# Kernel tuning notes

Measured on AMD Instinct MI355X. Metric: run time of the kernel, lower is better.

The kernel has to match this reference:

```python
import jax, jax.numpy as jnp
import numpy as np

L, D, DH, NH, P = 12, 768, 64, 12, 16
B, H_IMG, W_IMG = 16, 384, 384
MAX_GRID = 64


def setup_inputs() -> dict:
    key = jax.random.key(0)
    ks = jax.random.split(key, 10)
    r = lambda k, shp: (0.02 * jax.random.normal(k, shp, dtype=jnp.float32))
    return {
        "x": jax.random.normal(ks[0], (B, 3, H_IMG, W_IMG), dtype=jnp.float32),
        "conv_w": r(ks[1], (D, 3, P, P)),
        "conv_b": jnp.zeros((D,), jnp.float32),
        "ln_w": jnp.ones((D,), jnp.float32),
        "ln_b": jnp.zeros((D,), jnp.float32),
        "pos_y_emb": r(ks[2], (MAX_GRID, D)),
        "pos_x_emb": r(ks[3], (MAX_GRID, D)),
        "mha_ln_w": jnp.ones((L, D), jnp.float32),
        "mha_ln_b": jnp.zeros((L, D), jnp.float32),
        "qw": r(ks[4], (L, D, D)),
        "kw": r(ks[5], (L, D, D)),
        "vw": r(ks[6], (L, D, D)),
        "ffn_ln_w": jnp.ones((L, D), jnp.float32),
        "ffn_ln_b": jnp.zeros((L, D), jnp.float32),
        "w1": r(ks[7], (L, D, 4 * D)),
        "b1": jnp.zeros((L, 4 * D), jnp.float32),
        "w2": r(ks[8], (L, 4 * D, D)),
        "b2": jnp.zeros((L, D), jnp.float32),
        "x_shift": 0,
        "y_shift": 0,
    }


def _ln(x, w, b):
    m = jnp.mean(x, axis=-1, keepdims=True)
    v = jnp.var(x, axis=-1, keepdims=True)
    return (x - m) * jax.lax.rsqrt(v + 1e-5) * w + b


def reference(x, conv_w, conv_b, ln_w, ln_b, pos_y_emb, pos_x_emb,
              mha_ln_w, mha_ln_b, qw, kw, vw,
              ffn_ln_w, ffn_ln_b, w1, b1, w2, b2, x_shift, y_shift):
    # patch embed: conv + relu, to NHWC, layernorm
    h = jax.lax.conv_general_dilated(x, conv_w, (P, P), 'VALID',
                                     dimension_numbers=('NCHW', 'OIHW', 'NCHW'))
    h = jax.nn.relu(h + conv_b[None, :, None, None])
    h = jnp.transpose(h, (0, 2, 3, 1))  # [B, GH, GW, D]
    h = _ln(h, ln_w, ln_b)
    b, gh, gw, d = h.shape
    n = gh * gw
    # 2D factorized positional embedding, shared layernorm
    pos = (pos_y_emb[jnp.arange(gh) + y_shift][:, None, :]
           + pos_x_emb[jnp.arange(gw) + x_shift][None, :, :])  # [GH, GW, D]
    pos = _ln(pos, ln_w, ln_b).reshape(1, n, d)
    pos_emb = jnp.broadcast_to(pos, (b, n, d))
    t = h.reshape(b, n, d) + pos_emb
    scale = 1.0 / jnp.sqrt(jnp.float32(DH))
    for i in range(L):
        # pre-LN MHA (no output projection, mask=None / pretrain=False)
        tl = _ln(t, mha_ln_w[i], mha_ln_b[i])
        q = (tl @ qw[i]).reshape(b, n, NH, DH).transpose(0, 2, 1, 3)
        k = (tl @ kw[i]).reshape(b, n, NH, DH).transpose(0, 2, 1, 3)
        v = (tl @ vw[i]).reshape(b, n, NH, DH).transpose(0, 2, 1, 3)
        attn = jax.nn.softmax(jnp.einsum('bhqd,bhkd->bhqk', q, k) * scale, axis=-1)
        o = jnp.einsum('bhqk,bhkd->bhqd', attn, v).transpose(0, 2, 1, 3).reshape(b, n, d)
        t = t + o
        fl = _ln(t, ffn_ln_w[i], ffn_ln_b[i])
        t = t + (jax.nn.relu(fl @ w1[i] + b1[i]) @ w2[i] + b2[i])
    return t, pos_emb
```

## Files before the change

kernel.cpp:

```cpp
#include <hip/hip_runtime.h>

typedef unsigned short u16;
typedef __attribute__((ext_vector_type(4))) float f32x4;
typedef __attribute__((ext_vector_type(8))) short s16x8;

__device__ __forceinline__ u16 f2bf(float f) {
    union { float f; unsigned u; } v; v.f = f;
    unsigned r = v.u + 0x7FFFu + ((v.u >> 16) & 1u);
    return (u16)(r >> 16);
}

__device__ __forceinline__ void gload_lds16(const u16* g, u16* l) {
    __builtin_amdgcn_global_load_lds(
        (const __attribute__((address_space(1))) unsigned int*)(g),
        (__attribute__((address_space(3))) unsigned int*)(l),
        16, 0, 0);
}

#define NTOK 9216
#define SEQ  576
#define DMODEL 768
#define DFF  3072
#define NHEAD 12
#define HDIM 64

__global__ __launch_bounds__(256) void convert_bf16_kernel(const float* __restrict__ in,
                                                           u16* __restrict__ out, int n) {
    for (int i = blockIdx.x * 256 + threadIdx.x; i < n; i += gridDim.x * 256)
        out[i] = f2bf(in[i]);
}

__global__ __launch_bounds__(256) void copy_f32_kernel(const float* __restrict__ in,
                                                       float* __restrict__ out, int n4) {
    const float4* a = (const float4*)in;
    float4* o = (float4*)out;
    for (int i = blockIdx.x * 256 + threadIdx.x; i < n4; i += gridDim.x * 256)
        o[i] = a[i];
}

__global__ __launch_bounds__(256) void im2col_kernel(const float* __restrict__ x,
                                                     u16* __restrict__ out) {
    int tok = blockIdx.x;
    int b = tok / SEQ, n = tok % SEQ;
    int gy = n / 24, gx = n % 24;
    int tid = threadIdx.x;
#pragma unroll
    for (int j = 0; j < 3; ++j) {
        int col = tid + j * 256;
        int c = col >> 8, py = (col >> 4) & 15, px = col & 15;
        float v = x[(size_t)((b * 3 + c) * 384 + gy * 16 + py) * 384 + gx * 16 + px];
        out[(size_t)tok * DMODEL + col] = f2bf(v);
    }
}

__global__ __launch_bounds__(256) void transpose_layer_kernel(
        const float* __restrict__ qw, const float* __restrict__ kw, const float* __restrict__ vw,
        const float* __restrict__ w1, const float* __restrict__ w2,
        u16* __restrict__ wTq, u16* __restrict__ wTk, u16* __restrict__ wTv,
        u16* __restrict__ w1T, u16* __restrict__ w2T) {
    int bid = blockIdx.x;
    const float* src; u16* dst; int Kd, Nd, tile;
    if (bid < 1728)      { int m = bid / 576; src = m == 0 ? qw : (m == 1 ? kw : vw);
                           dst = m == 0 ? wTq : (m == 1 ? wTk : wTv); Kd = 768; Nd = 768; tile = bid % 576; }
    else if (bid < 4032) { src = w1; dst = w1T; Kd = 768; Nd = 3072; tile = bid - 1728; }
    else                 { src = w2; dst = w2T; Kd = 3072; Nd = 768; tile = bid - 4032; }
    int ntx = Nd / 32;
    int tk = (tile / ntx) * 32, tn = (tile % ntx) * 32;
    __shared__ float ts[32][33];
    int tx = threadIdx.x & 31, ty = threadIdx.x >> 5;
#pragma unroll
    for (int j = 0; j < 32; j += 8)
        ts[ty + j][tx] = src[(size_t)(tk + ty + j) * Nd + tn + tx];
    __syncthreads();
#pragma unroll
    for (int j = 0; j < 32; j += 8)
        dst[(size_t)(tn + ty + j) * Kd + tk + tx] = f2bf(ts[tx][ty + j]);
}

__global__ __launch_bounds__(256) void ln_bf16_kernel(const float* __restrict__ X,
                                                      const float* __restrict__ w,
                                                      const float* __restrict__ b,
                                                      u16* __restrict__ Y) {
    int row = blockIdx.x, tid = threadIdx.x;
    const float* x = X + (size_t)row * DMODEL;
    float v0 = x[tid], v1 = x[tid + 256], v2 = x[tid + 512];
    float s = v0 + v1 + v2, sq = v0 * v0 + v1 * v1 + v2 * v2;
#pragma unroll
    for (int off = 32; off >= 1; off >>= 1) { s += __shfl_down(s, off); sq += __shfl_down(sq, off); }
    __shared__ float red[8];
    if ((tid & 63) == 0) { red[tid >> 6] = s; red[4 + (tid >> 6)] = sq; }
    __syncthreads();
    float S = red[0] + red[1] + red[2] + red[3];
    float Q = red[4] + red[5] + red[6] + red[7];
    float mean = S * (1.f / DMODEL);
    float var = Q * (1.f / DMODEL) - mean * mean;
    float inv = rsqrtf(var + 1e-5f);
    u16* y = Y + (size_t)row * DMODEL;
    y[tid]       = f2bf((v0 - mean) * inv * w[tid]       + b[tid]);
    y[tid + 256] = f2bf((v1 - mean) * inv * w[tid + 256] + b[tid + 256]);
    y[tid + 512] = f2bf((v2 - mean) * inv * w[tid + 512] + b[tid + 512]);
}

__global__ __launch_bounds__(256) void ln_add_pos_kernel(float* __restrict__ T,
                                                         const float* __restrict__ w,
                                                         const float* __restrict__ b,
                                                         const float* __restrict__ posln) {
    int row = blockIdx.x, tid = threadIdx.x;
    float* x = T + (size_t)row * DMODEL;
    const float* p = posln + (size_t)(row % SEQ) * DMODEL;
    float v0 = x[tid], v1 = x[tid + 256], v2 = x[tid + 512];
    float s = v0 + v1 + v2, sq = v0 * v0 + v1 * v1 + v2 * v2;
#pragma unroll
    for (int off = 32; off >= 1; off >>= 1) { s += __shfl_down(s, off); sq += __shfl_down(sq, off); }
    __shared__ float red[8];
    if ((tid & 63) == 0) { red[tid >> 6] = s; red[4 + (tid >> 6)] = sq; }
    __syncthreads();
    float S = red[0] + red[1] + red[2] + red[3];
    float Q = red[4] + red[5] + red[6] + red[7];
    float mean = S * (1.f / DMODEL);
    float var = Q * (1.f / DMODEL) - mean * mean;
    float inv = rsqrtf(var + 1e-5f);
    x[tid]       = (v0 - mean) * inv * w[tid]       + b[tid]       + p[tid];
    x[tid + 256] = (v1 - mean) * inv * w[tid + 256] + b[tid + 256] + p[tid + 256];
    x[tid + 512] = (v2 - mean) * inv * w[tid + 512] + b[tid + 512] + p[tid + 512];
}

__global__ __launch_bounds__(256) void pos_ln_kernel(const float* __restrict__ py,
                                                     const float* __restrict__ px,
                                                     const float* __restrict__ w,
                                                     const float* __restrict__ b,
                                                     const int* __restrict__ xs_p,
                                                     const int* __restrict__ ys_p,
                                                     float* __restrict__ posln,
                                                     float* __restrict__ out2) {
    int row = blockIdx.x;
    int gy = row / 24, gx = row % 24;
    int ys = ys_p[0], xs = xs_p[0];
    int tid = threadIdx.x;
    float v[3]; float s = 0.f, sq = 0.f;
#pragma unroll
    for (int j = 0; j < 3; ++j) {
        int c = tid + j * 256;
        v[j] = py[(size_t)(gy + ys) * DMODEL + c] + px[(size_t)(gx + xs) * DMODEL + c];
        s += v[j]; sq += v[j] * v[j];
    }
#pragma unroll
    for (int off = 32; off >= 1; off >>= 1) { s += __shfl_down(s, off); sq += __shfl_down(sq, off); }
    __shared__ float red[8];
    if ((tid & 63) == 0) { red[tid >> 6] = s; red[4 + (tid >> 6)] = sq; }
    __syncthreads();
    float S = red[0] + red[1] + red[2] + red[3];
    float Q = red[4] + red[5] + red[6] + red[7];
    float mean = S * (1.f / DMODEL);
    float var = Q * (1.f / DMODEL) - mean * mean;
    float inv = rsqrtf(var + 1e-5f);
#pragma unroll
    for (int j = 0; j < 3; ++j) {
        int c = tid + j * 256;
        float y = (v[j] - mean) * inv * w[c] + b[c];
        posln[(size_t)row * DMODEL + c] = y;
        for (int bb = 0; bb < 16; ++bb)
            out2[((size_t)bb * SEQ + row) * DMODEL + c] = y;
    }
}

#define EPI_CONV 0
#define EPI_QKV  1
#define EPI_FFN1 3
#define EPI_FFN2 4

template <int EPI>
__global__ __launch_bounds__(512, 4) void gemm3b(const u16* __restrict__ A,
                                                 const u16* __restrict__ Bt,
                                                 float* __restrict__ outF,
                                                 u16* __restrict__ outB,
                                                 u16* __restrict__ outB2,
                                                 u16* __restrict__ outB3,
                                                 const float* __restrict__ bias,
                                                 int lda, int N, int K) {
    __shared__ __align__(16) u16 lds[3 * 12288];
    const int tid = threadIdx.x;
    const int wave = tid >> 6, lane = tid & 63;
    const int c_lo = lane & 15, c_hi = lane >> 4;
    const int wm = wave >> 2, wn = wave & 3;
    const int m0 = blockIdx.x * 128, n0 = blockIdx.y * 256;
    const int NT = K >> 5;

    const int srow = tid >> 2;
    const int koff = ((tid & 3) * 8) ^ (((srow >> 1) & 3) << 3);
    const u16* pA = A  + (size_t)(m0 + srow) * lda + koff;
    const u16* pB = Bt + (size_t)(n0 + srow) * lda + koff;
    const size_t rstepB = (size_t)128 * lda;
    f32x4 acc[4][4] = {};

    auto stage = [&](int t) {
        u16* buf = lds + (t % 3) * 12288;
        int k0 = t << 5;
        gload_lds16(pA + k0, buf + tid * 8);
        gload_lds16(pB + k0, buf + 4096 + tid * 8);
        gload_lds16(pB + rstepB + k0, buf + 8192 + tid * 8);
    };

    stage(0); stage(1);
    asm volatile("s_waitcnt vmcnt(3)" ::: "memory");
    __builtin_amdgcn_s_barrier();
    __builtin_amdgcn_sched_barrier(0);

    const int sw = ((c_lo >> 1) & 3) << 3;
    const int colA = (c_hi * 8) ^ sw;

    for (int t = 0; t < NT; ++t) {
        if (t + 2 < NT) stage(t + 2);
        const u16* buf = lds + (t % 3) * 12288;
        s16x8 af[4], bf[4];
#pragma unroll
        for (int m = 0; m < 4; ++m)
            af[m] = *(const s16x8*)(buf + (wm * 64 + m * 16 + c_lo) * 32 + colA);
#pragma unroll
        for (int n = 0; n < 4; ++n)
            bf[n] = *(const s16x8*)(buf + 4096 + (wn * 64 + n * 16 + c_lo) * 32 + colA);
        asm volatile("s_waitcnt lgkmcnt(0)" ::: "memory");
        __builtin_amdgcn_sched_barrier(0);
        __builtin_amdgcn_s_setprio(1);
#pragma unroll
        for (int m = 0; m < 4; ++m)
#pragma unroll
            for (int n = 0; n < 4; ++n)
                acc[m][n] = __builtin_amdgcn_mfma_f32_16x16x32_bf16(af[m], bf[n], acc[m][n], 0, 0, 0);
        __builtin_amdgcn_s_setprio(0);
        if (t + 2 < NT)      { asm volatile("s_waitcnt vmcnt(3)" ::: "memory"); }
        else if (t + 1 < NT) { asm volatile("s_waitcnt vmcnt(0)" ::: "memory"); }
        __builtin_amdgcn_s_barrier();
        __builtin_amdgcn_sched_barrier(0);
    }

#pragma unroll
    for (int mf = 0; mf < 4; ++mf)
#pragma unroll
        for (int nf = 0; nf < 4; ++nf)
#pragma unroll
            for (int rr = 0; rr < 4; ++rr) {
                int grow = m0 + wm * 64 + mf * 16 + c_hi * 4 + rr;
                int gcol = n0 + wn * 64 + nf * 16 + c_lo;
                float v = acc[mf][nf][rr];
                if (EPI == EPI_CONV) {
                    v += bias[gcol]; v = fmaxf(v, 0.f);
                    outF[(size_t)grow * 768 + gcol] = v;
                } else if (EPI == EPI_QKV) {
                    int sel = n0 / 768;
                    int lcol = gcol - sel * 768;
                    if (sel == 0)      outB [(size_t)grow * 768 + lcol] = f2bf(v);
                    else if (sel == 1) outB2[(size_t)grow * 768 + lcol] = f2bf(v);
                    else {
                        int b = grow / SEQ, nt = grow % SEQ;
                        int h = lcol >> 6, dh = lcol & 63;
                        outB3[(size_t)(((b * NHEAD + h) << 6) + dh) * SEQ + nt] = f2bf(v);
                    }
                } else if (EPI == EPI_FFN1) {
                    v += bias[gcol]; v = fmaxf(v, 0.f);
                    outB[(size_t)grow * N + gcol] = f2bf(v);
                } else if (EPI == EPI_FFN2) {
                    outF[(size_t)grow * 768 + gcol] += v + bias[gcol];
                }
            }
}

__global__ __launch_bounds__(256) void attn_kernel(const u16* __restrict__ Qb,
                                                   const u16* __restrict__ Kb,
                                                   const u16* __restrict__ Vt,
                                                   float* __restrict__ T) {
    int bid = blockIdx.x;
    int qt = bid / 192, bh = bid % 192;
    int b = bh / NHEAD, h = bh % NHEAD;
    int q0 = qt * 64;
    const int tid = threadIdx.x, wave = tid >> 6, lane = tid & 63;
    const int c_lo = lane & 15, c_hi = lane >> 4;
    __shared__ __align__(16) u16 Qs[64][72];
    __shared__ __align__(16) u16 Ks[64][72];
    __shared__ __align__(16) u16 Vs[64][72];
    __shared__ __align__(16) u16 Ps[4][16][72];
#pragma unroll
    for (int i = 0; i < 2; ++i) {
        int c = i * 256 + tid, row = c >> 3, slot = (c & 7) * 8;
        *(s16x8*)&Qs[row][slot] =
            *(const s16x8*)(Qb + ((size_t)(b * SEQ + q0 + row) * DMODEL + h * HDIM + slot));
    }
    s16x8 kreg[2], vreg[2];
    {
#pragma unroll
        for (int i = 0; i < 2; ++i) {
            int c = i * 256 + tid, row = c >> 3, slot = (c & 7) * 8;
            kreg[i] = *(const s16x8*)(Kb + ((size_t)(b * SEQ + row) * DMODEL + h * HDIM + slot));
            vreg[i] = *(const s16x8*)(Vt + ((size_t)((b * NHEAD + h) * HDIM + row) * SEQ + slot));
        }
    }
    f32x4 o[4] = {};
    float mrun[4], lrun[4];
#pragma unroll
    for (int r = 0; r < 4; ++r) { mrun[r] = -1e30f; lrun[r] = 0.f; }
    for (int t2 = 0; t2 < 9; ++t2) {
        __builtin_amdgcn_s_barrier();
#pragma unroll
        for (int i = 0; i < 2; ++i) {
            int c = i * 256 + tid, row = c >> 3, slot = (c & 7) * 8;
            *(s16x8*)&Ks[row][slot] = kreg[i];
            *(s16x8*)&Vs[row][slot] = vreg[i];
        }
        asm volatile("s_waitcnt lgkmcnt(0)" ::: "memory");
        __builtin_amdgcn_s_barrier();
        __builtin_amdgcn_sched_barrier(0);
        if (t2 < 8) {
            int kv0 = (t2 + 1) * 64;
#pragma unroll
            for (int i = 0; i < 2; ++i) {
                int c = i * 256 + tid, row = c >> 3, slot = (c & 7) * 8;
                kreg[i] = *(const s16x8*)(Kb + ((size_t)(b * SEQ + kv0 + row) * DMODEL + h * HDIM + slot));
                vreg[i] = *(const s16x8*)(Vt + ((size_t)((b * NHEAD + h) * HDIM + row) * SEQ + kv0 + slot));
            }
        }
        f32x4 s[4] = {};
        s16x8 aq[2];
#pragma unroll
        for (int ks = 0; ks < 2; ++ks)
            aq[ks] = *(const s16x8*)&Qs[wave * 16 + c_lo][ks * 32 + c_hi * 8];
#pragma unroll
        for (int nf = 0; nf < 4; ++nf)
#pragma unroll
            for (int ks = 0; ks < 2; ++ks) {
                s16x8 bk = *(const s16x8*)&Ks[nf * 16 + c_lo][ks * 32 + c_hi * 8];
                s[nf] = __builtin_amdgcn_mfma_f32_16x16x32_bf16(aq[ks], bk, s[nf], 0, 0, 0);
            }
#pragma unroll
        for (int nf = 0; nf < 4; ++nf)
#pragma unroll
            for (int r = 0; r < 4; ++r) s[nf][r] *= 0.125f;
        float mx[4];
#pragma unroll
        for (int r = 0; r < 4; ++r)
            mx[r] = fmaxf(fmaxf(s[0][r], s[1][r]), fmaxf(s[2][r], s[3][r]));
#pragma unroll
        for (int off = 1; off < 16; off <<= 1)
#pragma unroll
            for (int r = 0; r < 4; ++r) mx[r] = fmaxf(mx[r], __shfl_xor(mx[r], off));
        float alpha[4];
#pragma unroll
        for (int r = 0; r < 4; ++r) {
            float mn = fmaxf(mrun[r], mx[r]);
            alpha[r] = __expf(mrun[r] - mn);
            mrun[r] = mn;
            lrun[r] *= alpha[r];
        }
        float ls[4] = {0.f, 0.f, 0.f, 0.f};
        u16 pb[4][4];
#pragma unroll
        for (int nf = 0; nf < 4; ++nf)
#pragma unroll
            for (int r = 0; r < 4; ++r) {
                float p = __expf(s[nf][r] - mrun[r]);
                ls[r] += p;
                pb[nf][r] = f2bf(p);
            }
#pragma unroll
        for (int off = 1; off < 16; off <<= 1)
#pragma unroll
            for (int r = 0; r < 4; ++r) ls[r] += __shfl_xor(ls[r], off);
#pragma unroll
        for (int r = 0; r < 4; ++r) lrun[r] += ls[r];
#pragma unroll
        for (int df = 0; df < 4; ++df)
#pragma unroll
            for (int r = 0; r < 4; ++r) o[df][r] *= alpha[r];
#pragma unroll
        for (int nf = 0; nf < 4; ++nf)
#pragma unroll
            for (int r = 0; r < 4; ++r)
                Ps[wave][c_hi * 4 + r][c_lo + nf * 16] = pb[nf][r];
        asm volatile("s_waitcnt lgkmcnt(0)" ::: "memory");
        s16x8 pa[2];
#pragma unroll
        for (int ks = 0; ks < 2; ++ks)
            pa[ks] = *(const s16x8*)&Ps[wave][c_lo][ks * 32 + c_hi * 8];
#pragma unroll
        for (int df = 0; df < 4; ++df)
#pragma unroll
            for (int ks = 0; ks < 2; ++ks) {
                s16x8 bv = *(const s16x8*)&Vs[df * 16 + c_lo][ks * 32 + c_hi * 8];
                o[df] = __builtin_amdgcn_mfma_f32_16x16x32_bf16(pa[ks], bv, o[df], 0, 0, 0);
            }
    }
#pragma unroll
    for (int df = 0; df < 4; ++df)
#pragma unroll
        for (int r = 0; r < 4; ++r) {
            int grow = b * SEQ + q0 + wave * 16 + c_hi * 4 + r;
            int gcol = h * HDIM + df * 16 + c_lo;
            T[(size_t)grow * DMODEL + gcol] += o[df][r] / lrun[r];
        }
}

extern "C" void kernel_launch(void* const* d_in, const int* in_sizes, int n_in,
                              void* d_out, int out_size, void* d_ws, size_t ws_size,
                              hipStream_t stream) {
    (void)in_sizes; (void)n_in; (void)out_size; (void)ws_size;
    const float* x        = (const float*)d_in[0];
    const float* conv_w   = (const float*)d_in[1];
    const float* conv_b   = (const float*)d_in[2];
    const float* ln_w     = (const float*)d_in[3];
    const float* ln_b     = (const float*)d_in[4];
    const float* pos_y    = (const float*)d_in[5];
    const float* pos_x    = (const float*)d_in[6];
    const float* mha_ln_w = (const float*)d_in[7];
    const float* mha_ln_b = (const float*)d_in[8];
    const float* qw       = (const float*)d_in[9];
    const float* kw       = (const float*)d_in[10];
    const float* vw       = (const float*)d_in[11];
    const float* ffn_ln_w = (const float*)d_in[12];
    const float* ffn_ln_b = (const float*)d_in[13];
    const float* w1       = (const float*)d_in[14];
    const float* b1       = (const float*)d_in[15];
    const float* w2       = (const float*)d_in[16];
    const float* b2       = (const float*)d_in[17];
    const int*   xs       = (const int*)d_in[18];
    const int*   ys       = (const int*)d_in[19];
    float* out1 = (float*)d_out;
    float* out2 = out1 + (size_t)NTOK * DMODEL;

    size_t off = 0;
    char* ws = (char*)d_ws;
    auto carve = [&](size_t bytes) { char* p = ws + off; off += (bytes + 255) & ~(size_t)255; return p; };
    u16* wTqkv = (u16*)carve((size_t)3 * 768 * 768 * 2);
    u16* w1T = (u16*)carve((size_t)DFF * DMODEL * 2);
    u16* w2T = (u16*)carve((size_t)DMODEL * DFF * 2);
    float* t  = (float*)carve((size_t)NTOK * DMODEL * 4);
    u16* tl   = (u16*)carve((size_t)NTOK * DMODEL * 2);
    u16* qb   = (u16*)carve((size_t)NTOK * DMODEL * 2);
    u16* kb   = (u16*)carve((size_t)NTOK * DMODEL * 2);
    u16* vT   = (u16*)carve((size_t)NTOK * DMODEL * 2);
    u16* hb   = (u16*)carve((size_t)NTOK * DFF * 2);
    float* posln = (float*)carve((size_t)SEQ * DMODEL * 4);
    u16* wTq = wTqkv;
    u16* wTk = wTqkv + (size_t)768 * 768;
    u16* wTv = wTqkv + (size_t)2 * 768 * 768;
    u16* cw   = wTqkv;
    u16* im2c = hb;

    convert_bf16_kernel<<<1152, 256, 0, stream>>>(conv_w, cw, 768 * 768);
    im2col_kernel<<<NTOK, 256, 0, stream>>>(x, im2c);
    gemm3b<EPI_CONV><<<dim3(72, 3), 512, 0, stream>>>(im2c, cw, t, nullptr, nullptr, nullptr,
                                                      conv_b, 768, 768, 768);
    pos_ln_kernel<<<SEQ, 256, 0, stream>>>(pos_y, pos_x, ln_w, ln_b, xs, ys, posln, out2);
    ln_add_pos_kernel<<<NTOK, 256, 0, stream>>>(t, ln_w, ln_b, posln);

    for (int i = 0; i < 12; ++i) {
        transpose_layer_kernel<<<6336, 256, 0, stream>>>(
            qw + (size_t)i * 768 * 768, kw + (size_t)i * 768 * 768, vw + (size_t)i * 768 * 768,
            w1 + (size_t)i * 768 * DFF, w2 + (size_t)i * DFF * 768,
            wTq, wTk, wTv, w1T, w2T);
        ln_bf16_kernel<<<NTOK, 256, 0, stream>>>(t, mha_ln_w + i * DMODEL, mha_ln_b + i * DMODEL, tl);
        gemm3b<EPI_QKV><<<dim3(72, 9), 512, 0, stream>>>(tl, wTqkv, nullptr, qb, kb, vT,
                                                         nullptr, 768, 2304, 768);
        attn_kernel<<<16 * NHEAD * 9, 256, 0, stream>>>(qb, kb, vT, t);
        ln_bf16_kernel<<<NTOK, 256, 0, stream>>>(t, ffn_ln_w + i * DMODEL, ffn_ln_b + i * DMODEL, tl);
        gemm3b<EPI_FFN1><<<dim3(72, 12), 512, 0, stream>>>(tl, w1T, nullptr, hb, nullptr, nullptr,
                                                           b1 + (size_t)i * DFF, 768, 3072, 768);
        gemm3b<EPI_FFN2><<<dim3(72, 3), 512, 0, stream>>>(hb, w2T, t, nullptr, nullptr, nullptr,
                                                          b2 + (size_t)i * DMODEL, 3072, 768, 3072);
    }
    copy_f32_kernel<<<2048, 256, 0, stream>>>(t, out1, (NTOK * DMODEL) / 4);
}
```

Before: 3.206 ms.

## Hoist weight transpose into one launch; use 64x64 vectorised tiles and packed V stores

Weight transposition to bf16 now runs as a single launch over all 12 layers when the workspace is large enough, replacing twelve per-layer launches. A fallback keeps the per-layer path otherwise. The transpose kernel moves from 32x32 to 64x64 tiles with float4 loads and paired bf16 stores. The QKV GEMM epilogue writes the transposed V as packed 64-bit stores of four consecutive tokens instead of scattered 16-bit stores. The cost is more workspace to hold all layers' transposed weights.

```diff
diff --git a/kernel.cpp b/kernel.cpp
--- a/kernel.cpp
+++ b/kernel.cpp
@@ -53,28 +53,50 @@
     }
 }
 
-__global__ __launch_bounds__(256) void transpose_layer_kernel(
-        const float* __restrict__ qw, const float* __restrict__ kw, const float* __restrict__ vw,
-        const float* __restrict__ w1, const float* __restrict__ w2,
-        u16* __restrict__ wTq, u16* __restrict__ wTk, u16* __restrict__ wTv,
-        u16* __restrict__ w1T, u16* __restrict__ w2T) {
-    int bid = blockIdx.x;
+__global__ __launch_bounds__(256) void transpose64_kernel(
+        const float* __restrict__ qw0, const float* __restrict__ kw0, const float* __restrict__ vw0,
+        const float* __restrict__ w10, const float* __restrict__ w20,
+        u16* __restrict__ wTqkv0, u16* __restrict__ w1T0, u16* __restrict__ w2T0,
+        size_t wqkv_stride, size_t w1_stride) {
+    int layer = blockIdx.x / 1584;
+    int bid = blockIdx.x % 1584;
+    const float* qw = qw0 + (size_t)layer * 768 * 768;
+    const float* kw = kw0 + (size_t)layer * 768 * 768;
+    const float* vw = vw0 + (size_t)layer * 768 * 768;
+    const float* w1 = w10 + (size_t)layer * 768 * DFF;
+    const float* w2 = w20 + (size_t)layer * DFF * 768;
+    u16* wTq = wTqkv0 + (size_t)layer * wqkv_stride;
+    u16* wTk = wTq + (size_t)768 * 768;
+    u16* wTv = wTq + (size_t)2 * 768 * 768;
+    u16* w1T = w1T0 + (size_t)layer * w1_stride;
+    u16* w2T = w2T0 + (size_t)layer * w1_stride;
+
     const float* src; u16* dst; int Kd, Nd, tile;
-    if (bid < 1728)      { int m = bid / 576; src = m == 0 ? qw : (m == 1 ? kw : vw);
-                           dst = m == 0 ? wTq : (m == 1 ? wTk : wTv); Kd = 768; Nd = 768; tile = bid % 576; }
-    else if (bid < 4032) { src = w1; dst = w1T; Kd = 768; Nd = 3072; tile = bid - 1728; }
-    else                 { src = w2; dst = w2T; Kd = 3072; Nd = 768; tile = bid - 4032; }
-    int ntx = Nd / 32;
-    int tk = (tile / ntx) * 32, tn = (tile % ntx) * 32;
-    __shared__ float ts[32][33];
-    int tx = threadIdx.x & 31, ty = threadIdx.x >> 5;
-#pragma unroll
-    for (int j = 0; j < 32; j += 8)
-        ts[ty + j][tx] = src[(size_t)(tk + ty + j) * Nd + tn + tx];
+    if (bid < 432)       { int m = bid / 144; src = m == 0 ? qw : (m == 1 ? kw : vw);
+                           dst = m == 0 ? wTq : (m == 1 ? wTk : wTv); Kd = 768; Nd = 768; tile = bid % 144; }
+    else if (bid < 1008) { src = w1; dst = w1T; Kd = 768; Nd = 3072; tile = bid - 432; }
+    else                 { src = w2; dst = w2T; Kd = 3072; Nd = 768; tile = bid - 1008; }
+    int ntx = Nd >> 6;
+    int tk = (tile / ntx) << 6, tn = (tile % ntx) << 6;
+    __shared__ float ts[64][65];
+    int tx4 = threadIdx.x & 15, ty = threadIdx.x >> 4;
+#pragma unroll
+    for (int j = 0; j < 64; j += 16) {
+        float4 v = *(const float4*)&src[(size_t)(tk + ty + j) * Nd + tn + tx4 * 4];
+        ts[ty + j][tx4 * 4 + 0] = v.x;
+        ts[ty + j][tx4 * 4 + 1] = v.y;
+        ts[ty + j][tx4 * 4 + 2] = v.z;
+        ts[ty + j][tx4 * 4 + 3] = v.w;
+    }
     __syncthreads();
-#pragma unroll
-    for (int j = 0; j < 32; j += 8)
-        dst[(size_t)(tn + ty + j) * Kd + tk + tx] = f2bf(ts[tx][ty + j]);
+    int kx = threadIdx.x & 31, ry = threadIdx.x >> 5;
+#pragma unroll
+    for (int j = 0; j < 64; j += 8) {
+        int r = ry + j;
+        unsigned lo = f2bf(ts[2 * kx][r]);
+        unsigned hi = f2bf(ts[2 * kx + 1][r]);
+        *(unsigned*)&dst[(size_t)(tn + r) * Kd + tk + 2 * kx] = lo | (hi << 16);
+    }
 }
 
 __global__ __launch_bounds__(256) void ln_bf16_kernel(const float* __restrict__ X,
@@ -237,11 +259,24 @@
 #pragma unroll
     for (int mf = 0; mf < 4; ++mf)
 #pragma unroll
-        for (int nf = 0; nf < 4; ++nf)
+        for (int nf = 0; nf < 4; ++nf) {
+            int gcol = n0 + wn * 64 + nf * 16 + c_lo;
+            int tb = m0 + wm * 64 + mf * 16 + c_hi * 4;
+            if (EPI == EPI_QKV && (n0 / 768) == 2) {
+                int lcol = gcol - 2 * 768;
+                int b = tb / SEQ, nt = tb % SEQ;
+                int h = lcol >> 6, dh = lcol & 63;
+                unsigned long long pk =
+                    (unsigned long long)f2bf(acc[mf][nf][0])
+                    | ((unsigned long long)f2bf(acc[mf][nf][1]) << 16)
+                    | ((unsigned long long)f2bf(acc[mf][nf][2]) << 32)
+                    | ((unsigned long long)f2bf(acc[mf][nf][3]) << 48);
+                *(unsigned long long*)&outB3[(size_t)(((b * NHEAD + h) << 6) + dh) * SEQ + nt] = pk;
+                continue;
+            }
 #pragma unroll
             for (int rr = 0; rr < 4; ++rr) {
-                int grow = m0 + wm * 64 + mf * 16 + c_hi * 4 + rr;
-                int gcol = n0 + wn * 64 + nf * 16 + c_lo;
+                int grow = tb + rr;
                 float v = acc[mf][nf][rr];
                 if (EPI == EPI_CONV) {
                     v += bias[gcol]; v = fmaxf(v, 0.f);
@@ -250,12 +285,7 @@
                     int sel = n0 / 768;
                     int lcol = gcol - sel * 768;
                     if (sel == 0)      outB [(size_t)grow * 768 + lcol] = f2bf(v);
-                    else if (sel == 1) outB2[(size_t)grow * 768 + lcol] = f2bf(v);
-                    else {
-                        int b = grow / SEQ, nt = grow % SEQ;
-                        int h = lcol >> 6, dh = lcol & 63;
-                        outB3[(size_t)(((b * NHEAD + h) << 6) + dh) * SEQ + nt] = f2bf(v);
-                    }
+                    else               outB2[(size_t)grow * 768 + lcol] = f2bf(v);
                 } else if (EPI == EPI_FFN1) {
                     v += bias[gcol]; v = fmaxf(v, 0.f);
                     outB[(size_t)grow * N + gcol] = f2bf(v);
@@ -263,6 +293,7 @@
                     outF[(size_t)grow * 768 + gcol] += v + bias[gcol];
                 }
             }
+        }
 }
 
 __global__ __launch_bounds__(256) void attn_kernel(const u16* __restrict__ Qb,
@@ -401,7 +432,7 @@
 extern "C" void kernel_launch(void* const* d_in, const int* in_sizes, int n_in,
                               void* d_out, int out_size, void* d_ws, size_t ws_size,
                               hipStream_t stream) {
-    (void)in_sizes; (void)n_in; (void)out_size; (void)ws_size;
+    (void)in_sizes; (void)n_in; (void)out_size;
     const float* x        = (const float*)d_in[0];
     const float* conv_w   = (const float*)d_in[1];
     const float* conv_b   = (const float*)d_in[2];
@@ -428,9 +459,6 @@
     size_t off = 0;
     char* ws = (char*)d_ws;
     auto carve = [&](size_t bytes) { char* p = ws + off; off += (bytes + 255) & ~(size_t)255; return p; };
-    u16* wTqkv = (u16*)carve((size_t)3 * 768 * 768 * 2);
-    u16* w1T = (u16*)carve((size_t)DFF * DMODEL * 2);
-    u16* w2T = (u16*)carve((size_t)DMODEL * DFF * 2);
     float* t  = (float*)carve((size_t)NTOK * DMODEL * 4);
     u16* tl   = (u16*)carve((size_t)NTOK * DMODEL * 2);
     u16* qb   = (u16*)carve((size_t)NTOK * DMODEL * 2);
@@ -438,11 +466,16 @@
     u16* vT   = (u16*)carve((size_t)NTOK * DMODEL * 2);
     u16* hb   = (u16*)carve((size_t)NTOK * DFF * 2);
     float* posln = (float*)carve((size_t)SEQ * DMODEL * 4);
-    u16* wTq = wTqkv;
-    u16* wTk = wTqkv + (size_t)768 * 768;
-    u16* wTv = wTqkv + (size_t)2 * 768 * 768;
-    u16* cw   = wTqkv;
-    u16* im2c = hb;
+    const size_t QKV_STRIDE = (size_t)3 * 768 * 768;
+    const size_t W1_STRIDE  = (size_t)768 * DFF;
+    size_t need_all = off + (QKV_STRIDE + 2 * W1_STRIDE) * 12 * 2 + 4096;
+    bool hoist = (ws_size >= need_all);
+    int nl = hoist ? 12 : 1;
+    u16* wTqkv = (u16*)carve(QKV_STRIDE * nl * 2);
+    u16* w1T   = (u16*)carve(W1_STRIDE * nl * 2);
+    u16* w2T   = (u16*)carve(W1_STRIDE * nl * 2);
+    u16* cw    = wTqkv;
+    u16* im2c  = hb;
 
     convert_bf16_kernel<<<1152, 256, 0, stream>>>(conv_w, cw, 768 * 768);
     im2col_kernel<<<NTOK, 256, 0, stream>>>(x, im2c);
@@ -450,20 +483,27 @@
                                                       conv_b, 768, 768, 768);
     pos_ln_kernel<<<SEQ, 256, 0, stream>>>(pos_y, pos_x, ln_w, ln_b, xs, ys, posln, out2);
     ln_add_pos_kernel<<<NTOK, 256, 0, stream>>>(t, ln_w, ln_b, posln);
+    if (hoist)
+        transpose64_kernel<<<1584 * 12, 256, 0, stream>>>(qw, kw, vw, w1, w2,
+                                                          wTqkv, w1T, w2T, QKV_STRIDE, W1_STRIDE);
 
     for (int i = 0; i < 12; ++i) {
-        transpose_layer_kernel<<<6336, 256, 0, stream>>>(
-            qw + (size_t)i * 768 * 768, kw + (size_t)i * 768 * 768, vw + (size_t)i * 768 * 768,
-            w1 + (size_t)i * 768 * DFF, w2 + (size_t)i * DFF * 768,
-            wTq, wTk, wTv, w1T, w2T);
+        if (!hoist)
+            transpose64_kernel<<<1584, 256, 0, stream>>>(
+                qw + (size_t)i * 768 * 768, kw + (size_t)i * 768 * 768, vw + (size_t)i * 768 * 768,
+                w1 + (size_t)i * 768 * DFF, w2 + (size_t)i * DFF * 768,
+                wTqkv, w1T, w2T, 0, 0);
+        u16* wq = wTqkv + (hoist ? (size_t)i * QKV_STRIDE : 0) * 1;
+        u16* wf1 = w1T + (hoist ? (size_t)i * W1_STRIDE : 0);
+        u16* wf2 = w2T + (hoist ? (size_t)i * W1_STRIDE : 0);
         ln_bf16_kernel<<<NTOK, 256, 0, stream>>>(t, mha_ln_w + i * DMODEL, mha_ln_b + i * DMODEL, tl);
-        gemm3b<EPI_QKV><<<dim3(72, 9), 512, 0, stream>>>(tl, wTqkv, nullptr, qb, kb, vT,
+        gemm3b<EPI_QKV><<<dim3(72, 9), 512, 0, stream>>>(tl, wq, nullptr, qb, kb, vT,
                                                          nullptr, 768, 2304, 768);
         attn_kernel<<<16 * NHEAD * 9, 256, 0, stream>>>(qb, kb, vT, t);
         ln_bf16_kernel<<<NTOK, 256, 0, stream>>>(t, ffn_ln_w + i * DMODEL, ffn_ln_b + i * DMODEL, tl);
-        gemm3b<EPI_FFN1><<<dim3(72, 12), 512, 0, stream>>>(tl, w1T, nullptr, hb, nullptr, nullptr,
+        gemm3b<EPI_FFN1><<<dim3(72, 12), 512, 0, stream>>>(tl, wf1, nullptr, hb, nullptr, nullptr,
                                                            b1 + (size_t)i * DFF, 768, 3072, 768);
-        gemm3b<EPI_FFN2><<<dim3(72, 3), 512, 0, stream>>>(hb, w2T, t, nullptr, nullptr, nullptr,
+        gemm3b<EPI_FFN2><<<dim3(72, 3), 512, 0, stream>>>(hb, wf2, t, nullptr, nullptr, nullptr,
                                                           b2 + (size_t)i * DMODEL, 3072, 768, 3072);
     }
     copy_f32_kernel<<<2048, 256, 0, stream>>>(t, out1, (NTOK * DMODEL) / 4);
```

Result: faster. 3.110 ms (-3.0%).
